# Performance work log

Hardware: AMD Instinct MI355X
Metric: run time of the kernel (lower is better)

Reference implementation:

```python
import jax, jax.numpy as jnp
import numpy as np

N = 8192
H_DIM = 128
N_CLASSES = 10


def _cdist(a, b):
    # Euclidean distance matrix, torch.cdist(p=2) equivalent.
    d2 = (jnp.sum(a * a, axis=1)[:, None]
          + jnp.sum(b * b, axis=1)[None, :]
          - 2.0 * (a @ b.T))
    return jnp.sqrt(jnp.maximum(d2, 0.0))


def _adagae_regularization(distances, k):
    # Per-row sort-based adaptive-kernel thresholding (AdaGAE).
    sd = jnp.sort(distances, axis=1)            # [n, n]
    a = sd[:, k][:, None] + 1e-10               # k-th NN distance per row
    b = jnp.sum(sd[:, :k], axis=1)[:, None]     # sum of k nearest
    c = jax.nn.relu(a - distances)
    denom = a * k - b + 1e-10
    out = c / denom
    return (out + out.T) / 2.0


def _get_kernel(x, ohm_labels, sparsity):
    unknown = jnp.sum(ohm_labels, axis=1) == 0   # [n] bool
    known = ~unknown
    kk = known[:, None] & known[None, :]         # known-known region
    uu = unknown[:, None] & unknown[None, :]     # unknown-unknown region
    semantic = ohm_labels @ ohm_labels.T
    ed = _cdist(x, x)
    ed = (ed + ed.T) / 2.0
    adagae = _adagae_regularization(ed, sparsity)
    n_unknown = jnp.sum(unknown.astype(jnp.float32))
    fc = 1.0 / jnp.maximum(n_unknown, 1.0)       # heterogeneous fully-connected value
    kernel = jnp.where(kk, semantic, jnp.where(uu, adagae, fc))
    return kernel


def setup_inputs() -> dict:
    key = jax.random.key(0)
    k1, k2, k3 = jax.random.split(key, 3)
    x = jax.random.normal(k1, (N, H_DIM), dtype=jnp.float32)
    # labels in [0, N_CLASSES]; label == N_CLASSES -> unknown (all-zero one-hot row)
    labels = jax.random.randint(k2, (N,), 0, N_CLASSES + 1)
    ohm_labels = jnp.where((labels < N_CLASSES)[:, None],
                           jax.nn.one_hot(labels, N_CLASSES, dtype=jnp.float32),
                           0.0)
    W = jax.random.normal(k3, (2, H_DIM), dtype=jnp.float32) / np.sqrt(H_DIM)
    b = jnp.zeros((2,), dtype=jnp.float32)
    return {"x": x, "ohm_labels": ohm_labels, "W": W, "b": b, "spars": 32}


def reference(x, ohm_labels, W, b, spars):
    adj = _get_kernel(x, ohm_labels, spars)      # [n, n]
    h = x @ W.T + b                              # [n, 2]
    g = jnp.tanh(adj @ h)                        # [n, 2]
    # centroids (missing clusters stay zero)
    counts = jnp.sum(ohm_labels, axis=0)         # [n_classes]
    agg = ohm_labels.T @ g                       # [n_classes, 2]
    centroids = jnp.where((counts > 0)[:, None],
                          agg / jnp.maximum(counts, 1.0)[:, None], 0.0)
    scores = -_cdist(g, centroids)               # [n, n_classes]
    return scores, g, adj
```

## Files before the change

### kernel.cpp

```cpp
#include <hip/hip_runtime.h>
#include <hip/hip_bf16.h>
#include <math.h>

#define N 8192
#define D 128
#define NC 10

typedef float f4 __attribute__((ext_vector_type(4)));

__device__ __forceinline__ void nt_store4(float* p, float a, float b, float c, float d) {
    f4 v; v[0] = a; v[1] = b; v[2] = c; v[3] = d;
    __builtin_nontemporal_store(v, (f4*)p);
}


__global__ void k_zero(int* __restrict__ p) {
    if (threadIdx.x == 0) *p = 0;
}

__global__ void k_prep(const float* __restrict__ x, const float* __restrict__ ohm,
                       const float* __restrict__ W, const float* __restrict__ bb,
                       char* __restrict__ labs, float* __restrict__ nArr,
                       float* __restrict__ h, int* __restrict__ u_idx,
                       int* __restrict__ cpos, int* __restrict__ nuCnt) {
    int gt = blockIdx.x * blockDim.x + threadIdx.x;
    int wid = gt >> 6;
    int lane = gt & 63;
    if (wid >= N) return;
    const float2* xr = (const float2*)(x + (size_t)wid * D);
    float2 xv = xr[lane];
    float2 w0 = ((const float2*)W)[lane];
    float2 w1 = ((const float2*)(W + D))[lane];
    float nn = xv.x * xv.x + xv.y * xv.y;
    float h0 = xv.x * w0.x + xv.y * w0.y;
    float h1 = xv.x * w1.x + xv.y * w1.y;
    for (int off = 32; off; off >>= 1) {
        nn += __shfl_down(nn, off);
        h0 += __shfl_down(h0, off);
        h1 += __shfl_down(h1, off);
    }
    if (lane == 0) {
        nArr[wid] = nn;
        h[wid * 2 + 0] = h0 + bb[0];
        h[wid * 2 + 1] = h1 + bb[1];
        const float* orow = ohm + (size_t)wid * NC;
        int lab = -1;
        for (int c = 0; c < NC; ++c) {
            if (orow[c] > 0.5f) { lab = c; break; }
        }
        labs[wid] = (char)lab;
        if (lab < 0) {
            int slot = atomicAdd(nuCnt, 1);
            u_idx[slot] = wid;
            cpos[wid] = slot;
        }
    }
}

__global__ void k_sumA(const char* __restrict__ labs, const float* __restrict__ h,
                       float* __restrict__ part1) {
    __shared__ float L[256][33];
    int t = threadIdx.x;
    for (int s = 0; s < 33; ++s) L[t][s] = 0.f;
    int row = blockIdx.x * 256 + t;
    if (row < N) {
        int lab = labs[row];
        float h0 = h[row * 2], h1 = h[row * 2 + 1];
        if (lab >= 0) {
            L[t][lab * 2] = h0; L[t][lab * 2 + 1] = h1; L[t][22 + lab] = 1.f;
        } else {
            L[t][20] = h0; L[t][21] = h1; L[t][32] = 1.f;
        }
    }
    __syncthreads();
    if (t < 33) {
        float s = 0.f;
        for (int i = 0; i < 256; ++i) s += L[i][t];
        part1[blockIdx.x * 33 + t] = s;
    }
}

__global__ void k_sumB(const float* __restrict__ part1, float* __restrict__ scal) {
    int t = threadIdx.x;
    if (t < 33) {
        float s = 0.f;
        for (int i = 0; i < 64; ++i) s += part1[i * 33 + t];
        scal[t] = s;
    }
    __syncthreads();
    if (t == 0) {
        scal[33] = 1.0f / fmaxf(scal[32], 1.0f);
    }
}

__global__ void k_gemm(const float* __restrict__ x, const float* __restrict__ nArr,
                       const int* __restrict__ u_idx, const int* __restrict__ nuCnt,
                       int cap, float* __restrict__ d2a, float* __restrict__ adj) {
    __shared__ float As[64][D + 1];
    __shared__ float Bs[64][D + 1];
    __shared__ int Ai[64];
    int nu = *nuCnt;
    float* dst = (nu <= cap) ? d2a : adj;
    int t = threadIdx.x;
    int j0 = blockIdx.x * 64;
    for (int yy = blockIdx.y; yy * 64 < nu && yy < 128; yy += 12) {
        int a0 = yy * 64;
        if (yy != (int)blockIdx.y) __syncthreads();
        for (int c = t; c < 64 * 32; c += 256) {
            int r = c >> 5, c4 = c & 31;
            int a = a0 + r;
            int orig = (a < nu) ? u_idx[a] : u_idx[0];
            if (c4 == 0) Ai[r] = (a < nu) ? orig : -1;
            float4 av = ((const float4*)(x + (size_t)orig * D))[c4];
            As[r][c4 * 4 + 0] = av.x; As[r][c4 * 4 + 1] = av.y;
            As[r][c4 * 4 + 2] = av.z; As[r][c4 * 4 + 3] = av.w;
            float4 bv = ((const float4*)(x + (size_t)(j0 + r) * D))[c4];
            Bs[r][c4 * 4 + 0] = bv.x; Bs[r][c4 * 4 + 1] = bv.y;
            Bs[r][c4 * 4 + 2] = bv.z; Bs[r][c4 * 4 + 3] = bv.w;
        }
        __syncthreads();
        int tx = t & 15, ty = t >> 4;
        float acc[4][4];
#pragma unroll
        for (int m = 0; m < 4; ++m)
#pragma unroll
            for (int q = 0; q < 4; ++q) acc[m][q] = 0.f;
#pragma unroll 4
        for (int k = 0; k < D; ++k) {
            float a4[4], b4[4];
#pragma unroll
            for (int m = 0; m < 4; ++m) a4[m] = As[ty * 4 + m][k];
#pragma unroll
            for (int q = 0; q < 4; ++q) b4[q] = Bs[tx * 4 + q][k];
#pragma unroll
            for (int m = 0; m < 4; ++m)
#pragma unroll
                for (int q = 0; q < 4; ++q) acc[m][q] += a4[m] * b4[q];
        }
#pragma unroll
        for (int m = 0; m < 4; ++m) {
            int ar = ty * 4 + m;
            int orig = Ai[ar];
            if (orig < 0) continue;
            float ni = nArr[orig];
            int jb = j0 + tx * 4;
            float v0 = fmaxf(ni + nArr[jb + 0] - 2.f * acc[m][0], 0.f);
            float v1 = fmaxf(ni + nArr[jb + 1] - 2.f * acc[m][1], 0.f);
            float v2 = fmaxf(ni + nArr[jb + 2] - 2.f * acc[m][2], 0.f);
            float v3 = fmaxf(ni + nArr[jb + 3] - 2.f * acc[m][3], 0.f);
            if (orig == jb + 0) v0 = 0.f;
            if (orig == jb + 1) v1 = 0.f;
            if (orig == jb + 2) v2 = 0.f;
            if (orig == jb + 3) v3 = 0.f;
            float4 o; o.x = v0; o.y = v1; o.z = v2; o.w = v3;
            *((float4*)(dst + (size_t)(a0 + ar) * N + jb)) = o;
        }
    }
}

__global__ void k_self(const float* __restrict__ d2a, const float* __restrict__ adj_ro,
                       const int* __restrict__ u_idx, const int* __restrict__ nuCnt,
                       int cap, const int* __restrict__ spars,
                       const char* __restrict__ labs,
                       float* __restrict__ aArr, float* __restrict__ dinv,
                       float* __restrict__ adj) {
    __shared__ float wsf[4];
    __shared__ int wsi[8];
    int nu = *nuCnt;
    int t = threadIdx.x;
    int bid = blockIdx.x;
    if (bid >= 1024) {
        float fc = 1.0f / fmaxf((float)nu, 1.0f);
        int fb = bid - 1024;
        for (int rr = 0; rr < 4; ++rr) {
            int i = fb + 2048 * rr;
            int li = labs[i];
            if (li < 0) continue;
            float* row = adj + (size_t)i * N;
#pragma unroll
            for (int s = 0; s < 8; ++s) {
                int c4 = t + 256 * s;
                char4 l4 = ((const char4*)labs)[c4];
                float o0 = (l4.x < 0) ? fc : ((l4.x == li) ? 1.f : 0.f);
                float o1 = (l4.y < 0) ? fc : ((l4.y == li) ? 1.f : 0.f);
                float o2 = (l4.z < 0) ? fc : ((l4.z == li) ? 1.f : 0.f);
                float o3 = (l4.w < 0) ? fc : ((l4.w == li) ? 1.f : 0.f);
                nt_store4(row + c4 * 4, o0, o1, o2, o3);
            }
        }
        return;
    }
    const float* src = (nu <= cap) ? d2a : adj_ro;
    int k = *spars;
    int need = k + 1;
    int w = t >> 6;
    for (int rr = 0; rr < 8; ++rr) {
        int a = bid + 1024 * rr;
        if (a >= nu) break;
        const float4* rp = (const float4*)(src + (size_t)a * N);
        float v[32];
#pragma unroll
        for (int s = 0; s < 8; ++s) {
            float4 q = rp[t + 256 * s];
            v[s * 4 + 0] = q.x; v[s * 4 + 1] = q.y; v[s * 4 + 2] = q.z; v[s * 4 + 3] = q.w;
        }
        unsigned lo = 0u, hi = 0x7F800000u;
        for (int it = 0; it < 32; ++it) {
            unsigned mid = (lo + hi) >> 1;
            float mf = __uint_as_float(mid);
            int c = 0;
#pragma unroll
            for (int s = 0; s < 32; ++s) c += (v[s] <= mf) ? 1 : 0;
            for (int off = 32; off; off >>= 1) c += __shfl_down(c, off);
            if ((t & 63) == 0) wsi[(it & 1) * 4 + w] = c;
            __syncthreads();
            int base = (it & 1) * 4;
            c = wsi[base] + wsi[base + 1] + wsi[base + 2] + wsi[base + 3];
            if (lo < hi) {
                if (c >= need) hi = mid; else lo = mid + 1;
            }
        }
        float kvf = __uint_as_float(hi);
        float sum = 0.f; int clt = 0;
#pragma unroll
        for (int s = 0; s < 32; ++s) {
            if (v[s] < kvf) { clt++; sum += sqrtf(v[s]); }
        }
        for (int off = 32; off; off >>= 1) {
            sum += __shfl_down(sum, off);
            clt += __shfl_down(clt, off);
        }
        __syncthreads();
        if ((t & 63) == 0) { wsf[w] = sum; wsi[w] = clt; }
        __syncthreads();
        if (t == 0) {
            float sAll = wsf[0] + wsf[1] + wsf[2] + wsf[3];
            int cAll = wsi[0] + wsi[1] + wsi[2] + wsi[3];
            float skv = sqrtf(kvf);
            float aV = skv + 1e-10f;
            float b = sAll + (float)(k - cAll) * skv;
            float denom = aV * (float)k - b + 1e-10f;
            int orig = u_idx[a];
            aArr[orig] = aV;
            dinv[orig] = 1.0f / denom;
        }
        __syncthreads();
    }
}

__global__ void k_fu(const float* __restrict__ d2a, const char* __restrict__ labs,
                     const int* __restrict__ u_idx, const float* __restrict__ aArr,
                     const float* __restrict__ dinv, const float* __restrict__ h,
                     const int* __restrict__ nuCnt, int cap,
                     float* __restrict__ adj, float* __restrict__ gp) {
    __shared__ float red[256];
    int nu = *nuCnt;
    if (nu > cap) return;
    int t = threadIdx.x;
    int jc = blockIdx.x;
    float fc = 1.0f / fmaxf((float)nu, 1.0f);
    const float2* h2 = (const float2*)h;
    for (int a = blockIdx.y; a < nu; a += 768) {
        int i = u_idx[a];
        float ai = aArr[i], di = dinv[i];
        const float* drow = d2a + (size_t)a * N;
        float* orow = adj + (size_t)i * N;
        float s0 = 0.f, s1 = 0.f;
#pragma unroll
        for (int s = 0; s < 2; ++s) {
            int c4 = jc * 512 + s * 256 + t;
            int j = c4 * 4;
            float4 dv = ((const float4*)drow)[c4];
            char4 l4 = ((const char4*)labs)[c4];
            float dd[4] = {dv.x, dv.y, dv.z, dv.w};
            signed char ll[4] = {(signed char)l4.x, (signed char)l4.y,
                                 (signed char)l4.z, (signed char)l4.w};
            float v[4];
#pragma unroll
            for (int q = 0; q < 4; ++q) {
                if (ll[q] >= 0) {
                    v[q] = fc;
                } else {
                    float d = sqrtf(dd[q]);
                    v[q] = 0.5f * (fmaxf(ai - d, 0.f) * di
                                 + fmaxf(aArr[j + q] - d, 0.f) * dinv[j + q]);
                }
                float2 hh = h2[j + q];
                s0 += v[q] * hh.x;
                s1 += v[q] * hh.y;
            }
            nt_store4(orow + j, v[0], v[1], v[2], v[3]);
        }
        red[t] = s0; __syncthreads();
        for (int off = 128; off; off >>= 1) {
            if (t < off) red[t] += red[t + off];
            __syncthreads();
        }
        float r0 = red[0];
        __syncthreads();
        red[t] = s1; __syncthreads();
        for (int off = 128; off; off >>= 1) {
            if (t < off) red[t] += red[t + off];
            __syncthreads();
        }
        if (t == 0) { gp[a * 8 + jc * 2 + 0] = r0; gp[a * 8 + jc * 2 + 1] = red[0]; }
        __syncthreads();
    }
}

__global__ void k_fu_slow(const float* __restrict__ x, const float* __restrict__ nArr,
                          const int* __restrict__ u_idx, const int* __restrict__ nuCnt,
                          int cap, const char* __restrict__ labs,
                          const float* __restrict__ aArr, const float* __restrict__ dinv,
                          float* __restrict__ adj) {
    __shared__ float As[64][D + 1];
    __shared__ float Bs[64][D + 1];
    __shared__ int Ai[64];
    int nu = *nuCnt;
    if (nu <= cap) return;
    int t = threadIdx.x;
    float fc = 1.0f / fmaxf((float)nu, 1.0f);
    int j0 = blockIdx.x * 64;
    for (int yy = blockIdx.y; yy * 64 < nu && yy < 128; yy += 12) {
        int a0 = yy * 64;
        if (yy != (int)blockIdx.y) __syncthreads();
        for (int c = t; c < 64 * 32; c += 256) {
            int r = c >> 5, c4 = c & 31;
            int a = a0 + r;
            int orig = (a < nu) ? u_idx[a] : u_idx[0];
            if (c4 == 0) Ai[r] = (a < nu) ? orig : -1;
            float4 av = ((const float4*)(x + (size_t)orig * D))[c4];
            As[r][c4 * 4 + 0] = av.x; As[r][c4 * 4 + 1] = av.y;
            As[r][c4 * 4 + 2] = av.z; As[r][c4 * 4 + 3] = av.w;
            float4 bv = ((const float4*)(x + (size_t)(j0 + r) * D))[c4];
            Bs[r][c4 * 4 + 0] = bv.x; Bs[r][c4 * 4 + 1] = bv.y;
            Bs[r][c4 * 4 + 2] = bv.z; Bs[r][c4 * 4 + 3] = bv.w;
        }
        __syncthreads();
        int tx = t & 15, ty = t >> 4;
        float acc[4][4];
#pragma unroll
        for (int m = 0; m < 4; ++m)
#pragma unroll
            for (int q = 0; q < 4; ++q) acc[m][q] = 0.f;
#pragma unroll 4
        for (int k = 0; k < D; ++k) {
            float a4[4], b4[4];
#pragma unroll
            for (int m = 0; m < 4; ++m) a4[m] = As[ty * 4 + m][k];
#pragma unroll
            for (int q = 0; q < 4; ++q) b4[q] = Bs[tx * 4 + q][k];
#pragma unroll
            for (int m = 0; m < 4; ++m)
#pragma unroll
                for (int q = 0; q < 4; ++q) acc[m][q] += a4[m] * b4[q];
        }
#pragma unroll
        for (int m = 0; m < 4; ++m) {
            int ar = ty * 4 + m;
            int orig = Ai[ar];
            if (orig < 0) continue;
            float ni = nArr[orig];
            float ai = aArr[orig], di = dinv[orig];
            int jb = j0 + tx * 4;
            float4 o;
            float* op = (float*)&o;
#pragma unroll
            for (int q = 0; q < 4; ++q) {
                int j = jb + q;
                int lj = labs[j];
                float v;
                if (lj >= 0) {
                    v = fc;
                } else {
                    float d2 = fmaxf(ni + nArr[j] - 2.f * acc[m][q], 0.f);
                    if (orig == j) d2 = 0.f;
                    float d = sqrtf(d2);
                    v = 0.5f * (fmaxf(ai - d, 0.f) * di + fmaxf(aArr[j] - d, 0.f) * dinv[j]);
                }
                op[q] = v;
            }
            *((float4*)(adj + (size_t)orig * N + jb)) = o;
        }
    }
}

__global__ void k_gv(const float* __restrict__ adj, const float* __restrict__ h,
                     const int* __restrict__ u_idx, const int* __restrict__ nuCnt,
                     int cap, float* __restrict__ gpre) {
    __shared__ float red[256];
    int nu = *nuCnt;
    if (nu <= cap) return;
    int t = threadIdx.x;
    const float2* h2 = (const float2*)h;
    for (int rr = 0; rr < 8; ++rr) {
        int a = blockIdx.x + 1024 * rr;
        if (a >= nu) break;
        int orig = u_idx[a];
        const float4* row = (const float4*)(adj + (size_t)orig * N);
        float s0 = 0.f, s1 = 0.f;
#pragma unroll
        for (int s = 0; s < 8; ++s) {
            int c4 = t + 256 * s;
            float4 v = row[c4];
            int j = c4 * 4;
            float2 ha = h2[j + 0], hb = h2[j + 1], hc = h2[j + 2], hd = h2[j + 3];
            s0 += v.x * ha.x + v.y * hb.x + v.z * hc.x + v.w * hd.x;
            s1 += v.x * ha.y + v.y * hb.y + v.z * hc.y + v.w * hd.y;
        }
        red[t] = s0; __syncthreads();
        for (int off = 128; off; off >>= 1) {
            if (t < off) red[t] += red[t + off];
            __syncthreads();
        }
        if (t == 0) gpre[orig * 2 + 0] = red[0];
        __syncthreads();
        red[t] = s1; __syncthreads();
        for (int off = 128; off; off >>= 1) {
            if (t < off) red[t] += red[t + off];
            __syncthreads();
        }
        if (t == 0) gpre[orig * 2 + 1] = red[0];
        __syncthreads();
    }
}

__global__ void k_gagg(const char* __restrict__ labs, const float* __restrict__ gp,
                       const float* __restrict__ gpre, const int* __restrict__ cpos,
                       const int* __restrict__ nuCnt, int cap,
                       const float* __restrict__ scal, float* __restrict__ outg,
                       float* __restrict__ part2) {
    __shared__ float L[256][21];
    int nu = *nuCnt;
    int t = threadIdx.x;
    for (int s = 0; s < 20; ++s) L[t][s] = 0.f;
    int i = blockIdx.x * 256 + t;
    int li = labs[i];
    float fc = scal[33];
    float g0, g1;
    if (li >= 0) {
        g0 = scal[li * 2 + 0] + fc * scal[20];
        g1 = scal[li * 2 + 1] + fc * scal[21];
    } else if (nu <= cap) {
        int a = cpos[i];
        g0 = 0.f; g1 = 0.f;
#pragma unroll
        for (int jc = 0; jc < 4; ++jc) {
            g0 += gp[a * 8 + jc * 2 + 0];
            g1 += gp[a * 8 + jc * 2 + 1];
        }
    } else {
        g0 = gpre[i * 2 + 0];
        g1 = gpre[i * 2 + 1];
    }
    g0 = tanhf(g0); g1 = tanhf(g1);
    outg[i * 2 + 0] = g0;
    outg[i * 2 + 1] = g1;
    if (li >= 0) { L[t][li * 2 + 0] = g0; L[t][li * 2 + 1] = g1; }
    __syncthreads();
    if (t < 20) {
        float s = 0.f;
        for (int r = 0; r < 256; ++r) s += L[r][t];
        part2[blockIdx.x * 20 + t] = s;
    }
}

__global__ void k_scores(const float* __restrict__ g, const float* __restrict__ part2,
                         const float* __restrict__ scal, float* __restrict__ outs) {
    __shared__ float cent[20];
    int t = threadIdx.x;
    if (t < 20) {
        float s = 0.f;
        for (int i = 0; i < 32; ++i) s += part2[i * 20 + t];
        float cnt = scal[22 + (t >> 1)];
        cent[t] = (cnt > 0.f) ? s / fmaxf(cnt, 1.0f) : 0.f;
    }
    __syncthreads();
    int i = blockIdx.x * 256 + t;
    float g0 = g[i * 2 + 0], g1 = g[i * 2 + 1];
#pragma unroll
    for (int c = 0; c < NC; ++c) {
        float d0 = g0 - cent[c * 2 + 0];
        float d1 = g1 - cent[c * 2 + 1];
        outs[i * NC + c] = -sqrtf(d0 * d0 + d1 * d1);
    }
}

extern "C" void kernel_launch(void* const* d_in, const int* in_sizes, int n_in,
                              void* d_out, int out_size, void* d_ws, size_t ws_size,
                              hipStream_t stream) {
    const float* x = (const float*)d_in[0];
    const float* ohm = (const float*)d_in[1];
    const float* W = (const float*)d_in[2];
    const float* b = (const float*)d_in[3];
    const int* spars = (const int*)d_in[4];

    float* out = (float*)d_out;
    float* outScores = out;
    float* outG = out + (size_t)N * NC;
    float* adj = outG + (size_t)N * 2;

    char* wsb = (char*)d_ws;
    int* u_idx   = (int*)(wsb + 0);
    char* labs   = (char*)(wsb + 32768);
    float* nArr  = (float*)(wsb + 40960);
    float* aArr  = (float*)(wsb + 73728);
    float* dinv  = (float*)(wsb + 106496);
    float* hArr  = (float*)(wsb + 139264);
    float* gpre  = (float*)(wsb + 204800);
    float* part1 = (float*)(wsb + 270336);
    float* part2 = (float*)(wsb + 278784);
    float* scal  = (float*)(wsb + 283904);
    int* nuCnt   = (int*)(wsb + 284160);
    int* cpos    = (int*)(wsb + 335872);
    float* gp    = (float*)(wsb + 524288);
    float* d2a   = (float*)(wsb + 2097152);

    long capL = ((long)ws_size - 2097152L) / ((long)N * 4);
    if (capL < 0) capL = 0;
    if (capL > N) capL = N;
    int cap = (int)capL;
    bool mayFallback = (cap < N);

    k_zero<<<1, 64, 0, stream>>>(nuCnt);
    k_prep<<<2048, 256, 0, stream>>>(x, ohm, W, b, labs, nArr, hArr, u_idx, cpos, nuCnt);
    k_sumA<<<64, 256, 0, stream>>>(labs, hArr, part1);
    k_sumB<<<1, 64, 0, stream>>>(part1, scal);
    k_gemm<<<dim3(128, 12), 256, 0, stream>>>(x, nArr, u_idx, nuCnt, cap, d2a, adj);
    k_self<<<3072, 256, 0, stream>>>(d2a, adj, u_idx, nuCnt, cap, spars, labs,
                                     aArr, dinv, adj);
    k_fu<<<dim3(4, 768), 256, 0, stream>>>(d2a, labs, u_idx, aArr, dinv, hArr,
                                           nuCnt, cap, adj, gp);
    if (mayFallback) {
        k_fu_slow<<<dim3(128, 12), 256, 0, stream>>>(x, nArr, u_idx, nuCnt, cap, labs,
                                                     aArr, dinv, adj);
        k_gv<<<1024, 256, 0, stream>>>(adj, hArr, u_idx, nuCnt, cap, gpre);
    }
    k_gagg<<<32, 256, 0, stream>>>(labs, gp, gpre, cpos, nuCnt, cap, scal, outG, part2);
    k_scores<<<32, 256, 0, stream>>>(outG, part2, scal, outScores);
}
```

Before: 148.0 us.

## Fuse small setup and tail kernels and vectorize GEMM shared-memory tiles

Replaces the atomic-based unknown-row compaction with a single-block prefix scan that also computes the class sums. This removes k_zero, k_sumA and k_sumB, and merges k_gagg and k_scores into one single-block tail kernel, cutting several launches. The GEMM now stores and reads its shared-memory tiles as float4 with a 132-float row stride and a strided output mapping. The known-row fill in the fallback path moves into a separate kernel so that, when the fallback is taken, it runs after the fallback GEMM has written the adjacency. Single-block kernels serialize some work, and the compaction order becomes deterministic.

```diff
diff --git a/kernel.cpp b/kernel.cpp
--- a/kernel.cpp
+++ b/kernel.cpp
@@ -14,15 +14,10 @@
 }
 
 
-__global__ void k_zero(int* __restrict__ p) {
-    if (threadIdx.x == 0) *p = 0;
-}
-
 __global__ void k_prep(const float* __restrict__ x, const float* __restrict__ ohm,
                        const float* __restrict__ W, const float* __restrict__ bb,
                        char* __restrict__ labs, float* __restrict__ nArr,
-                       float* __restrict__ h, int* __restrict__ u_idx,
-                       int* __restrict__ cpos, int* __restrict__ nuCnt) {
+                       float* __restrict__ h) {
     int gt = blockIdx.x * blockDim.x + threadIdx.x;
     int wid = gt >> 6;
     int lane = gt & 63;
@@ -49,55 +44,59 @@
             if (orow[c] > 0.5f) { lab = c; break; }
         }
         labs[wid] = (char)lab;
-        if (lab < 0) {
-            int slot = atomicAdd(nuCnt, 1);
-            u_idx[slot] = wid;
-            cpos[wid] = slot;
-        }
-    }
-}
-
-__global__ void k_sumA(const char* __restrict__ labs, const float* __restrict__ h,
-                       float* __restrict__ part1) {
+    }
+}
+
+__global__ void k_sum(const char* __restrict__ labs, const float* __restrict__ h,
+                      float* __restrict__ scal, int* __restrict__ u_idx,
+                      int* __restrict__ cpos, int* __restrict__ nuCnt) {
     __shared__ float L[256][33];
+    __shared__ int pre[256];
     int t = threadIdx.x;
     for (int s = 0; s < 33; ++s) L[t][s] = 0.f;
-    int row = blockIdx.x * 256 + t;
-    if (row < N) {
+    int base = t * 32;
+    int myCnt = 0;
+    for (int r = 0; r < 32; ++r) {
+        int row = base + r;
         int lab = labs[row];
         float h0 = h[row * 2], h1 = h[row * 2 + 1];
         if (lab >= 0) {
-            L[t][lab * 2] = h0; L[t][lab * 2 + 1] = h1; L[t][22 + lab] = 1.f;
+            L[t][lab * 2] += h0; L[t][lab * 2 + 1] += h1; L[t][22 + lab] += 1.f;
         } else {
-            L[t][20] = h0; L[t][21] = h1; L[t][32] = 1.f;
-        }
-    }
+            L[t][20] += h0; L[t][21] += h1; myCnt++;
+        }
+    }
+    pre[t] = myCnt;
     __syncthreads();
-    if (t < 33) {
+    for (int off = 1; off < 256; off <<= 1) {
+        int v = (t >= off) ? pre[t - off] : 0;
+        __syncthreads();
+        pre[t] += v;
+        __syncthreads();
+    }
+    int nu = pre[255];
+    int slot = pre[t] - myCnt;
+    for (int r = 0; r < 32; ++r) {
+        int row = base + r;
+        if (labs[row] < 0) { u_idx[slot] = row; cpos[row] = slot; slot++; }
+    }
+    if (t == 0) *nuCnt = nu;
+    if (t < 32) {
         float s = 0.f;
         for (int i = 0; i < 256; ++i) s += L[i][t];
-        part1[blockIdx.x * 33 + t] = s;
-    }
-}
-
-__global__ void k_sumB(const float* __restrict__ part1, float* __restrict__ scal) {
-    int t = threadIdx.x;
-    if (t < 33) {
-        float s = 0.f;
-        for (int i = 0; i < 64; ++i) s += part1[i * 33 + t];
         scal[t] = s;
     }
-    __syncthreads();
     if (t == 0) {
-        scal[33] = 1.0f / fmaxf(scal[32], 1.0f);
+        scal[32] = (float)nu;
+        scal[33] = 1.0f / fmaxf((float)nu, 1.0f);
     }
 }
 
 __global__ void k_gemm(const float* __restrict__ x, const float* __restrict__ nArr,
                        const int* __restrict__ u_idx, const int* __restrict__ nuCnt,
                        int cap, float* __restrict__ d2a, float* __restrict__ adj) {
-    __shared__ float As[64][D + 1];
-    __shared__ float Bs[64][D + 1];
+    __shared__ float As[64][132];
+    __shared__ float Bs[64][132];
     __shared__ int Ai[64];
     int nu = *nuCnt;
     float* dst = (nu <= cap) ? d2a : adj;
@@ -112,11 +111,9 @@
             int orig = (a < nu) ? u_idx[a] : u_idx[0];
             if (c4 == 0) Ai[r] = (a < nu) ? orig : -1;
             float4 av = ((const float4*)(x + (size_t)orig * D))[c4];
-            As[r][c4 * 4 + 0] = av.x; As[r][c4 * 4 + 1] = av.y;
-            As[r][c4 * 4 + 2] = av.z; As[r][c4 * 4 + 3] = av.w;
+            *(float4*)&As[r][c4 * 4] = av;
             float4 bv = ((const float4*)(x + (size_t)(j0 + r) * D))[c4];
-            Bs[r][c4 * 4 + 0] = bv.x; Bs[r][c4 * 4 + 1] = bv.y;
-            Bs[r][c4 * 4 + 2] = bv.z; Bs[r][c4 * 4 + 3] = bv.w;
+            *(float4*)&Bs[r][c4 * 4] = bv;
         }
         __syncthreads();
         int tx = t & 15, ty = t >> 4;
@@ -126,34 +123,32 @@
 #pragma unroll
             for (int q = 0; q < 4; ++q) acc[m][q] = 0.f;
 #pragma unroll 4
-        for (int k = 0; k < D; ++k) {
-            float a4[4], b4[4];
-#pragma unroll
-            for (int m = 0; m < 4; ++m) a4[m] = As[ty * 4 + m][k];
-#pragma unroll
-            for (int q = 0; q < 4; ++q) b4[q] = Bs[tx * 4 + q][k];
+        for (int k4 = 0; k4 < 32; ++k4) {
+            float4 a4[4], b4[4];
+#pragma unroll
+            for (int m = 0; m < 4; ++m) a4[m] = *(const float4*)&As[ty + 16 * m][k4 * 4];
+#pragma unroll
+            for (int q = 0; q < 4; ++q) b4[q] = *(const float4*)&Bs[tx + 16 * q][k4 * 4];
 #pragma unroll
             for (int m = 0; m < 4; ++m)
 #pragma unroll
-                for (int q = 0; q < 4; ++q) acc[m][q] += a4[m] * b4[q];
+                for (int q = 0; q < 4; ++q)
+                    acc[m][q] += a4[m].x * b4[q].x + a4[m].y * b4[q].y
+                               + a4[m].z * b4[q].z + a4[m].w * b4[q].w;
         }
 #pragma unroll
         for (int m = 0; m < 4; ++m) {
-            int ar = ty * 4 + m;
+            int ar = ty + 16 * m;
             int orig = Ai[ar];
             if (orig < 0) continue;
             float ni = nArr[orig];
-            int jb = j0 + tx * 4;
-            float v0 = fmaxf(ni + nArr[jb + 0] - 2.f * acc[m][0], 0.f);
-            float v1 = fmaxf(ni + nArr[jb + 1] - 2.f * acc[m][1], 0.f);
-            float v2 = fmaxf(ni + nArr[jb + 2] - 2.f * acc[m][2], 0.f);
-            float v3 = fmaxf(ni + nArr[jb + 3] - 2.f * acc[m][3], 0.f);
-            if (orig == jb + 0) v0 = 0.f;
-            if (orig == jb + 1) v1 = 0.f;
-            if (orig == jb + 2) v2 = 0.f;
-            if (orig == jb + 3) v3 = 0.f;
-            float4 o; o.x = v0; o.y = v1; o.z = v2; o.w = v3;
-            *((float4*)(dst + (size_t)(a0 + ar) * N + jb)) = o;
+#pragma unroll
+            for (int q = 0; q < 4; ++q) {
+                int j = j0 + tx + 16 * q;
+                float v = fmaxf(ni + nArr[j] - 2.f * acc[m][q], 0.f);
+                if (orig == j) v = 0.f;
+                dst[(size_t)(a0 + ar) * N + j] = v;
+            }
         }
     }
 }
@@ -170,6 +165,7 @@
     int t = threadIdx.x;
     int bid = blockIdx.x;
     if (bid >= 1024) {
+        if (nu > cap) return;
         float fc = 1.0f / fmaxf((float)nu, 1.0f);
         int fb = bid - 1024;
         for (int rr = 0; rr < 4; ++rr) {
@@ -305,6 +301,31 @@
         }
         if (t == 0) { gp[a * 8 + jc * 2 + 0] = r0; gp[a * 8 + jc * 2 + 1] = red[0]; }
         __syncthreads();
+    }
+}
+
+__global__ void k_fill_known_fb(const char* __restrict__ labs,
+                                const int* __restrict__ nuCnt, int cap,
+                                float* __restrict__ adj) {
+    int nu = *nuCnt;
+    if (nu <= cap) return;
+    int t = threadIdx.x;
+    float fc = 1.0f / fmaxf((float)nu, 1.0f);
+    for (int rr = 0; rr < 4; ++rr) {
+        int i = blockIdx.x + 2048 * rr;
+        int li = labs[i];
+        if (li < 0) continue;
+        float* row = adj + (size_t)i * N;
+#pragma unroll
+        for (int s = 0; s < 8; ++s) {
+            int c4 = t + 256 * s;
+            char4 l4 = ((const char4*)labs)[c4];
+            float o0 = (l4.x < 0) ? fc : ((l4.x == li) ? 1.f : 0.f);
+            float o1 = (l4.y < 0) ? fc : ((l4.y == li) ? 1.f : 0.f);
+            float o2 = (l4.z < 0) ? fc : ((l4.z == li) ? 1.f : 0.f);
+            float o3 = (l4.w < 0) ? fc : ((l4.w == li) ? 1.f : 0.f);
+            nt_store4(row + c4 * 4, o0, o1, o2, o3);
+        }
     }
 }
 
@@ -425,64 +446,54 @@
     }
 }
 
-__global__ void k_gagg(const char* __restrict__ labs, const float* __restrict__ gp,
+__global__ void k_tail(const char* __restrict__ labs, const float* __restrict__ gp,
                        const float* __restrict__ gpre, const int* __restrict__ cpos,
                        const int* __restrict__ nuCnt, int cap,
                        const float* __restrict__ scal, float* __restrict__ outg,
-                       float* __restrict__ part2) {
+                       float* __restrict__ outs) {
     __shared__ float L[256][21];
+    __shared__ float cent[20];
     int nu = *nuCnt;
     int t = threadIdx.x;
     for (int s = 0; s < 20; ++s) L[t][s] = 0.f;
-    int i = blockIdx.x * 256 + t;
-    int li = labs[i];
     float fc = scal[33];
-    float g0, g1;
-    if (li >= 0) {
-        g0 = scal[li * 2 + 0] + fc * scal[20];
-        g1 = scal[li * 2 + 1] + fc * scal[21];
-    } else if (nu <= cap) {
-        int a = cpos[i];
-        g0 = 0.f; g1 = 0.f;
-#pragma unroll
-        for (int jc = 0; jc < 4; ++jc) {
-            g0 += gp[a * 8 + jc * 2 + 0];
-            g1 += gp[a * 8 + jc * 2 + 1];
-        }
-    } else {
-        g0 = gpre[i * 2 + 0];
-        g1 = gpre[i * 2 + 1];
-    }
-    g0 = tanhf(g0); g1 = tanhf(g1);
-    outg[i * 2 + 0] = g0;
-    outg[i * 2 + 1] = g1;
-    if (li >= 0) { L[t][li * 2 + 0] = g0; L[t][li * 2 + 1] = g1; }
+    for (int rr = 0; rr < 32; ++rr) {
+        int i = rr * 256 + t;
+        int li = labs[i];
+        float g0, g1;
+        if (li >= 0) {
+            g0 = scal[li * 2 + 0] + fc * scal[20];
+            g1 = scal[li * 2 + 1] + fc * scal[21];
+        } else if (nu <= cap) {
+            int a = cpos[i];
+            g0 = gp[a * 8 + 0] + gp[a * 8 + 2] + gp[a * 8 + 4] + gp[a * 8 + 6];
+            g1 = gp[a * 8 + 1] + gp[a * 8 + 3] + gp[a * 8 + 5] + gp[a * 8 + 7];
+        } else {
+            g0 = gpre[i * 2 + 0];
+            g1 = gpre[i * 2 + 1];
+        }
+        g0 = tanhf(g0); g1 = tanhf(g1);
+        outg[i * 2 + 0] = g0;
+        outg[i * 2 + 1] = g1;
+        if (li >= 0) { L[t][li * 2 + 0] += g0; L[t][li * 2 + 1] += g1; }
+    }
     __syncthreads();
     if (t < 20) {
         float s = 0.f;
         for (int r = 0; r < 256; ++r) s += L[r][t];
-        part2[blockIdx.x * 20 + t] = s;
-    }
-}
-
-__global__ void k_scores(const float* __restrict__ g, const float* __restrict__ part2,
-                         const float* __restrict__ scal, float* __restrict__ outs) {
-    __shared__ float cent[20];
-    int t = threadIdx.x;
-    if (t < 20) {
-        float s = 0.f;
-        for (int i = 0; i < 32; ++i) s += part2[i * 20 + t];
         float cnt = scal[22 + (t >> 1)];
         cent[t] = (cnt > 0.f) ? s / fmaxf(cnt, 1.0f) : 0.f;
     }
     __syncthreads();
-    int i = blockIdx.x * 256 + t;
-    float g0 = g[i * 2 + 0], g1 = g[i * 2 + 1];
-#pragma unroll
-    for (int c = 0; c < NC; ++c) {
-        float d0 = g0 - cent[c * 2 + 0];
-        float d1 = g1 - cent[c * 2 + 1];
-        outs[i * NC + c] = -sqrtf(d0 * d0 + d1 * d1);
+    for (int rr = 0; rr < 32; ++rr) {
+        int i = rr * 256 + t;
+        float g0 = outg[i * 2 + 0], g1 = outg[i * 2 + 1];
+#pragma unroll
+        for (int c = 0; c < NC; ++c) {
+            float d0 = g0 - cent[c * 2 + 0];
+            float d1 = g1 - cent[c * 2 + 1];
+            outs[i * NC + c] = -sqrtf(d0 * d0 + d1 * d1);
+        }
     }
 }
 
@@ -508,8 +519,6 @@
     float* dinv  = (float*)(wsb + 106496);
     float* hArr  = (float*)(wsb + 139264);
     float* gpre  = (float*)(wsb + 204800);
-    float* part1 = (float*)(wsb + 270336);
-    float* part2 = (float*)(wsb + 278784);
     float* scal  = (float*)(wsb + 283904);
     int* nuCnt   = (int*)(wsb + 284160);
     int* cpos    = (int*)(wsb + 335872);
@@ -522,20 +531,19 @@
     int cap = (int)capL;
     bool mayFallback = (cap < N);
 
-    k_zero<<<1, 64, 0, stream>>>(nuCnt);
-    k_prep<<<2048, 256, 0, stream>>>(x, ohm, W, b, labs, nArr, hArr, u_idx, cpos, nuCnt);
-    k_sumA<<<64, 256, 0, stream>>>(labs, hArr, part1);
-    k_sumB<<<1, 64, 0, stream>>>(part1, scal);
+    k_prep<<<2048, 256, 0, stream>>>(x, ohm, W, b, labs, nArr, hArr);
+    k_sum<<<1, 256, 0, stream>>>(labs, hArr, scal, u_idx, cpos, nuCnt);
     k_gemm<<<dim3(128, 12), 256, 0, stream>>>(x, nArr, u_idx, nuCnt, cap, d2a, adj);
     k_self<<<3072, 256, 0, stream>>>(d2a, adj, u_idx, nuCnt, cap, spars, labs,
                                      aArr, dinv, adj);
     k_fu<<<dim3(4, 768), 256, 0, stream>>>(d2a, labs, u_idx, aArr, dinv, hArr,
                                            nuCnt, cap, adj, gp);
     if (mayFallback) {
+        k_fill_known_fb<<<2048, 256, 0, stream>>>(labs, nuCnt, cap, adj);
         k_fu_slow<<<dim3(128, 12), 256, 0, stream>>>(x, nArr, u_idx, nuCnt, cap, labs,
                                                      aArr, dinv, adj);
         k_gv<<<1024, 256, 0, stream>>>(adj, hArr, u_idx, nuCnt, cap, gpre);
     }
-    k_gagg<<<32, 256, 0, stream>>>(labs, gp, gpre, cpos, nuCnt, cap, scal, outG, part2);
-    k_scores<<<32, 256, 0, stream>>>(outG, part2, scal, outScores);
-}
+    k_tail<<<1, 256, 0, stream>>>(labs, gp, gpre, cpos, nuCnt, cap, scal,
+                                  outG, outScores);
+}
```

Result: slower. 201.1 us (+35.9%).
